# Optimization experiments

Measured on AMD Instinct MI355X. Metric: run time of the kernel, lower is better.

Reference implementation:

```python
import jax, jax.numpy as jnp
import numpy as np

OUT = 14          # output_size of mask_roi_pool
RATIO = 2         # sampling_ratio
SCALES = (0.25, 0.125, 0.0625, 0.03125)  # strides 4,8,16,32 for 800x800 images
CANON_SCALE = 224.0
CANON_LVL = 4.0
K_MIN = 2.0       # -log2(0.25)
K_MAX = 5.0


def setup_inputs() -> dict:
    key = jax.random.key(0)
    ks = jax.random.split(key, 8)
    B, N, C = 2, 128, 256
    feats = {}
    for i, hw in enumerate([200, 100, 50, 25]):
        feats[f"feat{i}"] = jax.random.normal(ks[i], (B, C, hw, hw), dtype=jnp.float32)
    # valid xyxy boxes in [0,800] with log-uniform sizes spanning all FPN levels
    img = 800.0
    logw = jax.random.uniform(ks[4], (B, N), minval=jnp.log(16.0), maxval=jnp.log(600.0))
    logh = jax.random.uniform(ks[5], (B, N), minval=jnp.log(16.0), maxval=jnp.log(600.0))
    w, h = jnp.exp(logw), jnp.exp(logh)
    x1 = jax.random.uniform(ks[6], (B, N)) * (img - w)
    y1 = jax.random.uniform(ks[7], (B, N)) * (img - h)
    boxes = jnp.stack([x1, y1, x1 + w, y1 + h], axis=-1).astype(jnp.float32)
    feats["boxes"] = boxes
    return feats


def _prep_axis(c, L):
    # torchvision roi_align bilinear clamp semantics (aligned=False)
    valid = (c > -1.0) & (c < L)
    c = jnp.clip(c, 0.0, L - 1.0)
    lo = jnp.clip(jnp.floor(c), 0.0, L - 2.0).astype(jnp.int32)
    frac = c - lo.astype(c.dtype)
    return valid, lo, frac


def _roi_align_level(feat, rois, bidx, scale):
    # feat: [B,C,H,W], rois: [K,4] xyxy image coords, bidx: [K] int32
    B, C, H, W = feat.shape
    K = rois.shape[0]
    x1 = rois[:, 0] * scale
    y1 = rois[:, 1] * scale
    x2 = rois[:, 2] * scale
    y2 = rois[:, 3] * scale
    rw = jnp.maximum(x2 - x1, 1.0)
    rh = jnp.maximum(y2 - y1, 1.0)
    bw = rw / OUT
    bh = rh / OUT
    # sample offsets within roi in bin units: (ph*RATIO + iy + 0.5)/RATIO, flattened [OUT*RATIO]
    off = (jnp.arange(OUT * RATIO, dtype=feat.dtype) + 0.5) / RATIO
    ys = y1[:, None] + bh[:, None] * off  # [K, 28]
    xs = x1[:, None] + bw[:, None] * off  # [K, 28]
    vy, ylo, ly = _prep_axis(ys, H)
    vx, xlo, lx = _prep_axis(xs, W)
    hy, hx = 1.0 - ly, 1.0 - lx
    feat_r = feat.transpose(0, 2, 3, 1).reshape(B * H * W, C)
    base = bidx[:, None, None] * (H * W)

    def gather(yi, xi):
        idx = base + yi[:, :, None] * W + xi[:, None, :]  # [K,28,28]
        return feat_r[idx]  # [K,28,28,C]

    val = (gather(ylo, xlo) * (hy[:, :, None] * hx[:, None, :])[..., None]
           + gather(ylo, xlo + 1) * (hy[:, :, None] * lx[:, None, :])[..., None]
           + gather(ylo + 1, xlo) * (ly[:, :, None] * hx[:, None, :])[..., None]
           + gather(ylo + 1, xlo + 1) * (ly[:, :, None] * lx[:, None, :])[..., None])
    mask = (vy[:, :, None] & vx[:, None, :])[..., None]
    val = jnp.where(mask, val, 0.0)
    # average RATIO x RATIO samples per output bin
    val = val.reshape(K, OUT, RATIO, OUT, RATIO, C).mean(axis=(2, 4))
    return val.transpose(0, 3, 1, 2)  # [K, C, OUT, OUT]


def _forward(feat0, feat1, feat2, feat3, boxes):
    feats = (feat0, feat1, feat2, feat3)
    B, N = boxes.shape[0], boxes.shape[1]
    rois = boxes.reshape(B * N, 4)
    bidx = jnp.repeat(jnp.arange(B, dtype=jnp.int32), N)
    # FPN level mapper (torchvision LevelMapper)
    w = rois[:, 2] - rois[:, 0]
    h = rois[:, 3] - rois[:, 1]
    s = jnp.sqrt(w * h)
    lvl = jnp.floor(CANON_LVL + jnp.log2(s / CANON_SCALE + 1e-6))
    lvl_idx = (jnp.clip(lvl, K_MIN, K_MAX) - K_MIN).astype(jnp.int32)  # [K] in 0..3
    per_level = jnp.stack(
        [_roi_align_level(f, rois, bidx, sc) for f, sc in zip(feats, SCALES)]
    )  # [4, K, C, 14, 14]
    K = rois.shape[0]
    return per_level[lvl_idx, jnp.arange(K)]  # [K, C, 14, 14]


def reference(feat0, feat1, feat2, feat3, boxes):
    return _forward(feat0, feat1, feat2, feat3, boxes)
```

## Files before the change

### kernel.cpp

```cpp
#include <hip/hip_runtime.h>
#include <math.h>

#define OUT 14
#define RATIO 2
#define NS (OUT*RATIO)
#define NPIX (OUT*OUT)
#define C_TOT 256
#define CG 4
#define NBOX_PER_B 128
#define NTHREADS 256
#define PATCH_CAP 1280
#define NROI 256

__device__ __forceinline__ void prep_axis(float c, int L, int& lo, float& fh, float& fl)
{
    const bool  v  = (c > -1.0f) && (c < (float)L);
    const float cc = fminf(fmaxf(c, 0.0f), (float)(L - 1));
    const float fb = fminf(fmaxf(floorf(cc), 0.0f), (float)(L - 2));
    const float fr = cc - fb;
    lo = (int)fb;
    fl = v ? fr        : 0.0f;
    fh = v ? 1.0f - fr : 0.0f;
}

__device__ __forceinline__ int axis_lo(float c, int L)
{
    const float cc = fminf(fmaxf(c, 0.0f), (float)(L - 1));
    return (int)fminf(fmaxf(floorf(cc), 0.0f), (float)(L - 2));
}

__global__ __launch_bounds__(NTHREADS)
void roi_align_fused_kernel(const float* __restrict__ f0,
                            const float* __restrict__ f1,
                            const float* __restrict__ f2,
                            const float* __restrict__ f3,
                            const float* __restrict__ boxes,
                            float* __restrict__ out)
{
    const int cg  = blockIdx.x;
    const int k   = blockIdx.y;
    const int tid = threadIdx.x;

    __shared__ float4 s_patch[PATCH_CAP];

    const float bx1 = boxes[k*4+0];
    const float by1 = boxes[k*4+1];
    const float bx2 = boxes[k*4+2];
    const float by2 = boxes[k*4+3];

    const float wbox = bx2 - bx1;
    const float hbox = by2 - by1;
    const float sdim = sqrtf(wbox * hbox);
    float lvlf = floorf(4.0f + log2f(sdim / 224.0f + 1e-6f));
    lvlf = fminf(fmaxf(lvlf, 2.0f), 5.0f);
    const int lidx = (int)lvlf - 2;

    const float* fptr;
    int H, W;
    float scale;
    if      (lidx == 0) { fptr = f0; H = 200; W = 200; scale = 0.25f;    }
    else if (lidx == 1) { fptr = f1; H = 100; W = 100; scale = 0.125f;   }
    else if (lidx == 2) { fptr = f2; H = 50;  W = 50;  scale = 0.0625f;  }
    else                { fptr = f3; H = 25;  W = 25;  scale = 0.03125f; }

    const float x1 = bx1 * scale;
    const float y1 = by1 * scale;
    const float x2 = bx2 * scale;
    const float y2 = by2 * scale;
    const float rw = fmaxf(x2 - x1, 1.0f);
    const float rh = fmaxf(y2 - y1, 1.0f);
    const float bw = rw / (float)OUT;
    const float bh = rh / (float)OUT;

    const float off0  = 0.25f;
    const float offL  = ((float)(NS-1) + 0.5f) * 0.5f;
    const int ymin  = axis_lo(y1 + bh * off0, H);
    const int xmin  = axis_lo(x1 + bw * off0, W);
    const int nrows = axis_lo(y1 + bh * offL, H) + 2 - ymin;
    const int ncols = axis_lo(x1 + bw * offL, W) + 2 - xmin;
    const int padded  = ncols | 1;
    const int stridep = (nrows * padded <= PATCH_CAP) ? padded : ncols;
    const int nelem   = nrows * ncols;
    const float rcpc  = 1.0f / (float)ncols;

    const bool active = (tid < NPIX);
    int rb0 = 0, rb1 = 0, cb0 = 0, cb1 = 0;
    float4 wy = {0,0,0,0};
    float4 wx = {0,0,0,0};
    if (active) {
        const int ph = tid / OUT;
        const int pw = tid - ph * OUT;
        int lo; float fh, fl;
        prep_axis(y1 + bh * (((float)(2*ph)   + 0.5f) * 0.5f), H, lo, fh, fl);
        rb0 = (lo - ymin) * stridep; wy.x = fh * 0.25f; wy.y = fl * 0.25f;
        prep_axis(y1 + bh * (((float)(2*ph+1) + 0.5f) * 0.5f), H, lo, fh, fl);
        rb1 = (lo - ymin) * stridep; wy.z = fh * 0.25f; wy.w = fl * 0.25f;
        prep_axis(x1 + bw * (((float)(2*pw)   + 0.5f) * 0.5f), W, lo, fh, fl);
        cb0 = lo - xmin; wx.x = fh; wx.y = fl;
        prep_axis(x1 + bw * (((float)(2*pw+1) + 0.5f) * 0.5f), W, lo, fh, fl);
        cb1 = lo - xmin; wx.z = fh; wx.w = fl;
    }

    const size_t plane = (size_t)H * (size_t)W;
    const float* fbase = fptr
        + ((size_t)(k / NBOX_PER_B) * C_TOT + (size_t)cg * CG) * plane
        + (size_t)ymin * W + xmin;
    const float* g0 = fbase;
    const float* g1 = fbase +   plane;
    const float* g2 = fbase + 2*plane;
    const float* g3 = fbase + 3*plane;
    for (int i = tid; i < nelem; i += NTHREADS) {
        const int r  = (int)(((float)i + 0.5f) * rcpc);
        const int cc = i - r * ncols;
        const int go = r * W + cc;
        const int di = r * stridep + cc;
        float4 v;
        v.x = g0[go]; v.y = g1[go]; v.z = g2[go]; v.w = g3[go];
        if (di < PATCH_CAP) s_patch[di] = v;
    }
    __syncthreads();

    if (active) {
        float4 acc = {0.0f, 0.0f, 0.0f, 0.0f};
        #pragma unroll
        for (int ys = 0; ys < 2; ++ys) {
            const int   rb = ys ? rb1 : rb0;
            const float yh = ys ? wy.z : wy.x;
            const float yl = ys ? wy.w : wy.y;
            #pragma unroll
            for (int xs = 0; xs < 2; ++xs) {
                const int base = rb + (xs ? cb1 : cb0);
                const float xh = xs ? wx.z : wx.x;
                const float xl = xs ? wx.w : wx.y;
                const float w00 = yh*xh, w01 = yh*xl, w10 = yl*xh, w11 = yl*xl;
                const float4 v00 = s_patch[base];
                const float4 v01 = s_patch[base + 1];
                const float4 v10 = s_patch[base + stridep];
                const float4 v11 = s_patch[base + stridep + 1];
                acc.x += w00*v00.x + w01*v01.x + w10*v10.x + w11*v11.x;
                acc.y += w00*v00.y + w01*v01.y + w10*v10.y + w11*v11.y;
                acc.z += w00*v00.z + w01*v01.z + w10*v10.z + w11*v11.z;
                acc.w += w00*v00.w + w01*v01.w + w10*v10.w + w11*v11.w;
            }
        }
        float* ob = out + ((size_t)k * C_TOT + (size_t)cg * CG) * NPIX + tid;
        ob[0*NPIX] = acc.x;
        ob[1*NPIX] = acc.y;
        ob[2*NPIX] = acc.z;
        ob[3*NPIX] = acc.w;
    }
}

extern "C" void kernel_launch(void* const* d_in, const int* in_sizes, int n_in,
                              void* d_out, int out_size, void* d_ws, size_t ws_size,
                              hipStream_t stream) {
    const float* f0    = (const float*)d_in[0];
    const float* f1    = (const float*)d_in[1];
    const float* f2    = (const float*)d_in[2];
    const float* f3    = (const float*)d_in[3];
    const float* boxes = (const float*)d_in[4];
    float* out = (float*)d_out;

    dim3 grid(C_TOT / CG, NROI);
    roi_align_fused_kernel<<<grid, NTHREADS, 0, stream>>>(f0, f1, f2, f3, boxes, out);
}
```

Before: 40.72 us.

## Process two channel groups per block and precompute patch load indices

```diff
diff --git a/kernel.cpp b/kernel.cpp
--- a/kernel.cpp
+++ b/kernel.cpp
@@ -7,9 +7,12 @@
 #define NPIX (OUT*OUT)
 #define C_TOT 256
 #define CG 4
+#define GPB 2
+#define NCHUNK (C_TOT/(CG*GPB))
 #define NBOX_PER_B 128
 #define NTHREADS 256
 #define PATCH_CAP 1280
+#define MAXIT 5
 #define NROI 256
 
 __device__ __forceinline__ void prep_axis(float c, int L, int& lo, float& fh, float& fl)
@@ -30,16 +33,16 @@
 }
 
 __global__ __launch_bounds__(NTHREADS)
-void roi_align_fused_kernel(const float* __restrict__ f0,
-                            const float* __restrict__ f1,
-                            const float* __restrict__ f2,
-                            const float* __restrict__ f3,
-                            const float* __restrict__ boxes,
-                            float* __restrict__ out)
+void roi_align_fused2_kernel(const float* __restrict__ f0,
+                             const float* __restrict__ f1,
+                             const float* __restrict__ f2,
+                             const float* __restrict__ f3,
+                             const float* __restrict__ boxes,
+                             float* __restrict__ out)
 {
-    const int cg  = blockIdx.x;
-    const int k   = blockIdx.y;
-    const int tid = threadIdx.x;
+    const int chunk = blockIdx.x;
+    const int k     = blockIdx.y;
+    const int tid   = threadIdx.x;
 
     __shared__ float4 s_patch[PATCH_CAP];
 
@@ -102,52 +105,68 @@
     }
 
     const size_t plane = (size_t)H * (size_t)W;
-    const float* fbase = fptr
-        + ((size_t)(k / NBOX_PER_B) * C_TOT + (size_t)cg * CG) * plane
-        + (size_t)ymin * W + xmin;
-    const float* g0 = fbase;
-    const float* g1 = fbase +   plane;
-    const float* g2 = fbase + 2*plane;
-    const float* g3 = fbase + 3*plane;
-    for (int i = tid; i < nelem; i += NTHREADS) {
+    int go_[MAXIT], di_[MAXIT];
+    #pragma unroll
+    for (int t = 0; t < MAXIT; ++t) {
+        const int i  = t*NTHREADS + tid;
         const int r  = (int)(((float)i + 0.5f) * rcpc);
         const int cc = i - r * ncols;
-        const int go = r * W + cc;
-        const int di = r * stridep + cc;
-        float4 v;
-        v.x = g0[go]; v.y = g1[go]; v.z = g2[go]; v.w = g3[go];
-        if (di < PATCH_CAP) s_patch[di] = v;
+        go_[t] = r * W + cc;
+        di_[t] = (i < nelem && r * stridep + cc < PATCH_CAP) ? (r * stridep + cc) : -1;
     }
-    __syncthreads();
 
-    if (active) {
-        float4 acc = {0.0f, 0.0f, 0.0f, 0.0f};
+    const float* fbase = fptr
+        + ((size_t)(k / NBOX_PER_B) * C_TOT + (size_t)chunk * (GPB*CG)) * plane
+        + (size_t)ymin * W + xmin;
+    float* outk = out + ((size_t)k * C_TOT + (size_t)chunk * (GPB*CG)) * NPIX;
+
+    #pragma unroll
+    for (int g = 0; g < GPB; ++g) {
+        const float* g0 = fbase + (size_t)(g*CG) * plane;
+        const float* g1 = g0 +   plane;
+        const float* g2 = g0 + 2*plane;
+        const float* g3 = g0 + 3*plane;
         #pragma unroll
-        for (int ys = 0; ys < 2; ++ys) {
-            const int   rb = ys ? rb1 : rb0;
-            const float yh = ys ? wy.z : wy.x;
-            const float yl = ys ? wy.w : wy.y;
-            #pragma unroll
-            for (int xs = 0; xs < 2; ++xs) {
-                const int base = rb + (xs ? cb1 : cb0);
-                const float xh = xs ? wx.z : wx.x;
-                const float xl = xs ? wx.w : wx.y;
-                const float w00 = yh*xh, w01 = yh*xl, w10 = yl*xh, w11 = yl*xl;
-                const float4 v00 = s_patch[base];
-                const float4 v01 = s_patch[base + 1];
-                const float4 v10 = s_patch[base + stridep];
-                const float4 v11 = s_patch[base + stridep + 1];
-                acc.x += w00*v00.x + w01*v01.x + w10*v10.x + w11*v11.x;
-                acc.y += w00*v00.y + w01*v01.y + w10*v10.y + w11*v11.y;
-                acc.z += w00*v00.z + w01*v01.z + w10*v10.z + w11*v11.z;
-                acc.w += w00*v00.w + w01*v01.w + w10*v10.w + w11*v11.w;
+        for (int t = 0; t < MAXIT; ++t) {
+            if (di_[t] >= 0) {
+                const int go = go_[t];
+                float4 v;
+                v.x = g0[go]; v.y = g1[go]; v.z = g2[go]; v.w = g3[go];
+                s_patch[di_[t]] = v;
             }
         }
-        float* ob = out + ((size_t)k * C_TOT + (size_t)cg * CG) * NPIX + tid;
-        ob[0*NPIX] = acc.x;
-        ob[1*NPIX] = acc.y;
-        ob[2*NPIX] = acc.z;
-        ob[3*NPIX] = acc.w;
+        __syncthreads();
+
+        if (active) {
+            float4 acc = {0.0f, 0.0f, 0.0f, 0.0f};
+            #pragma unroll
+            for (int ys = 0; ys < 2; ++ys) {
+                const int   rb = ys ? rb1 : rb0;
+                const float yh = ys ? wy.z : wy.x;
+                const float yl = ys ? wy.w : wy.y;
+                #pragma unroll
+                for (int xs = 0; xs < 2; ++xs) {
+                    const int base = rb + (xs ? cb1 : cb0);
+                    const float xh = xs ? wx.z : wx.x;
+                    const float xl = xs ? wx.w : wx.y;
+                    const float w00 = yh*xh, w01 = yh*xl, w10 = yl*xh, w11 = yl*xl;
+                    const float4 v00 = s_patch[base];
+                    const float4 v01 = s_patch[base + 1];
+                    const float4 v10 = s_patch[base + stridep];
+                    const float4 v11 = s_patch[base + stridep + 1];
+                    acc.x += w00*v00.x + w01*v01.x + w10*v10.x + w11*v11.x;
+                    acc.y += w00*v00.y + w01*v01.y + w10*v10.y + w11*v11.y;
+                    acc.z += w00*v00.z + w01*v01.z + w10*v10.z + w11*v11.z;
+                    acc.w += w00*v00.w + w01*v01.w + w10*v10.w + w11*v11.w;
+                }
+            }
+            float* ob = outk + (size_t)(g*CG) * NPIX + tid;
+            ob[0*NPIX] = acc.x;
+            ob[1*NPIX] = acc.y;
+            ob[2*NPIX] = acc.z;
+            ob[3*NPIX] = acc.w;
+        }
+        if (g + 1 < GPB) __syncthreads();
     }
 }
 
@@ -161,6 +180,6 @@
     const float* boxes = (const float*)d_in[4];
     float* out = (float*)d_out;
 
-    dim3 grid(C_TOT / CG, NROI);
-    roi_align_fused_kernel<<<grid, NTHREADS, 0, stream>>>(f0, f1, f2, f3, boxes, out);
+    dim3 grid(NCHUNK, NROI);
+    roi_align_fused2_kernel<<<grid, NTHREADS, 0, stream>>>(f0, f1, f2, f3, boxes, out);
 }
```

Result: faster. 37.37 us (-8.2%).
